# Optimization experiments

Hardware: AMD Instinct MI355X
Metric: run time of the kernel (lower is better)

The kernel has to match this reference:

```python
import jax, jax.numpy as jnp
import numpy as np

NUM_HEADS = 16
HEAD_DIM = 64
MEMORY_SIZE = 65536
K_SIMILAR = 8
K_CONTIGUOUS = 2
SURPRISE_THRESHOLD = 0.5
EPS = 1e-8  # torch F.cosine_similarity eps


def setup_inputs() -> dict:
    key = jax.random.key(0)
    ks = jax.random.split(key, 6)
    B, H, S, HD = 4, NUM_HEADS, 8192, HEAD_DIM
    D = H * HD
    inputs = jax.random.normal(ks[0], (B, S, D), dtype=jnp.float32)
    q = jax.random.normal(ks[1], (B, H, S, HD), dtype=jnp.float32)
    k = jax.random.normal(ks[2], (B, H, S, HD), dtype=jnp.float32)
    v = jax.random.normal(ks[3], (B, H, S, HD), dtype=jnp.float32)
    attention_mask = jnp.ones((B, S), dtype=jnp.float32)
    events = jax.random.normal(ks[4], (MEMORY_SIZE, D), dtype=jnp.float32)
    return {"inputs": inputs, "q": q, "k": k, "v": v,
            "attention_mask": attention_mask, "events": events,
            "seq_len_q": 8192}


def _segment_mean(kf, seg, S):
    # kf: [S, D], seg: [S] int32 segment ids (exclusive cumsum of boundary mask)
    sums = jax.ops.segment_sum(kf, seg, num_segments=S)          # [S, D]
    cnts = jax.ops.segment_sum(jnp.ones_like(seg, jnp.float32), seg, num_segments=S)
    means = sums / jnp.maximum(cnts, 1.0)[:, None]
    return means, cnts


def reference(inputs, q, k, v, attention_mask, events, seq_len_q):
    B, H, S, HD = k.shape
    D = H * HD
    # flatten keys per token: [B, S, H*HD]
    kf = k.transpose(0, 2, 1, 3).reshape(B, S, D)

    # --- surprise scores: ||k_t - k_{t-1}|| padded with 0 at t=0 ---
    diffs = kf[:, 1:] - kf[:, :-1]
    norms = jnp.linalg.norm(diffs, axis=-1)                      # [B, S-1]
    surprise = jnp.pad(norms, ((0, 0), (1, 0)))                  # [B, S]

    # --- event segmentation (threshold = mean + c*std, unbiased std like torch) ---
    mean = jnp.mean(surprise, axis=1, keepdims=True)
    std = jnp.std(surprise, axis=1, ddof=1, keepdims=True)
    bmask = surprise > (mean + SURPRISE_THRESHOLD * std)
    bmask = bmask.at[:, -1].set(True)                            # last index is always a boundary
    bi = bmask.astype(jnp.int32)
    seg = jnp.cumsum(bi, axis=1) - bi                            # token t -> #boundaries before t

    # --- memory update: mean-pool keys within each event (scatter) ---
    new_events, event_lengths = jax.vmap(_segment_mean, in_axes=(0, 0, None))(kf, seg, S)
    # new_events: [B, S, D] (rows >= num_events are zero), event_lengths: [B, S]

    # --- retrieval: cosine sim of last-token key vs memory, top-k gather ---
    query = kf[:, -1]                                            # [B, D]
    qn = jnp.maximum(jnp.linalg.norm(query, axis=-1), EPS)       # [B]
    en = jnp.maximum(jnp.linalg.norm(events, axis=-1), EPS)      # [M]
    sims = (query @ events.T) / (qn[:, None] * en[None, :])      # [B, M]
    kt = min(K_SIMILAR + K_CONTIGUOUS, events.shape[0])
    _, idx = jax.lax.top_k(sims, kt)                             # [B, kt]

    ret = events[idx]                                            # [B, kt, D]
    ret = ret.reshape(B, kt, H, HD).transpose(0, 2, 1, 3)        # [B, H, kt, HD]
    ret_k, ret_v = ret, ret                                      # non-differential: v == k slice

    aug_k = jnp.concatenate([ret_k, k], axis=2)                  # [B, H, kt+S, HD]
    aug_v = jnp.concatenate([ret_v, v], axis=2)
    aug_mask = jnp.concatenate([jnp.ones((B, kt), attention_mask.dtype), attention_mask], axis=1)

    cp = seq_len_q - 1
    ret_pos = jnp.linspace(float(cp - kt), float(cp - 1), kt, dtype=jnp.float32)
    pos = jnp.arange(S, dtype=jnp.float32)
    aug_positions = jnp.broadcast_to(jnp.concatenate([ret_pos, pos]), (B, kt + S))

    return (inputs, q, aug_k, aug_v, aug_mask, aug_positions, new_events, event_lengths)
```

## Files before the change

### kernel.cpp

```cpp
#include <hip/hip_runtime.h>
#include <math.h>

#define BB 4
#define HH 16
#define SS 8192
#define HDD 64
#define DD 1024
#define MEM 65536
#define KT 10
#define AUGROWS (SS + KT)

static const long O0 = 0;
static const long O1 = 33554432;
static const long O2 = 67108864;
static const long O3 = 100704256;
static const long O4 = 134299648;
static const long O5 = 134332456;
static const long O6 = 134365264;
static const long O7 = 167919696;

#define WS_NEED_FUSED 5767168UL

#define N4REG 8388608L

typedef float __attribute__((ext_vector_type(4))) f4v;

static __device__ __forceinline__ void nt_store4(float4* p, float4 v) {
    f4v t; t.x = v.x; t.y = v.y; t.z = v.z; t.w = v.w;
    __builtin_nontemporal_store(t, (f4v*)p);
}
static __device__ __forceinline__ float4 nt_load4(const float4* p) {
    f4v t = __builtin_nontemporal_load((const f4v*)p);
    float4 v; v.x = t.x; v.y = t.y; v.z = t.z; v.w = t.w;
    return v;
}

#define COPY_BLOCKS 4096
#define SIMS_BLOCKS 4096
__global__ __launch_bounds__(256) void bigfused_kernel(
        const float4* __restrict__ in0, const float4* __restrict__ q,
        const float4* __restrict__ k4, const float4* __restrict__ v,
        const float4* __restrict__ events4, float4* __restrict__ out4,
        double* __restrict__ partial, float* __restrict__ sims, int do_part) {
    __shared__ float4 qls4[BB][256];
    int blk = blockIdx.x;
    int tid = threadIdx.x;
    if (blk < COPY_BLOCKS) {
        int band = blk >> 10;
        long i = ((long)(blk & 1023)) * 256 + tid;
        const long bstride = 1024L * 256;
        if (band == 0) {
            for (; i < N4REG; i += bstride)
                nt_store4(out4 + (O0 >> 2) + i, nt_load4(in0 + i));
        } else if (band == 1) {
            for (; i < N4REG; i += bstride)
                nt_store4(out4 + (O1 >> 2) + i, nt_load4(q + i));
        } else if (band == 3) {
            for (; i < N4REG; i += bstride) {
                long chunk = i >> 17;
                long r = i & 131071;
                nt_store4(out4 + (O3 >> 2) + chunk * 131232L + 160 + r,
                          nt_load4(v + i));
            }
        } else {
            for (; i < N4REG; i += bstride) {
                long chunk = i >> 17;
                long r = i & 131071;
                float4 cur = k4[i];
                out4[(O2 >> 2) + chunk * 131232L + 160 + r] = cur;
                if (do_part) {
                    int s = (int)(r >> 4);
                    if (s > 0) {
                        float4 pv = k4[i - 16];
                        double dx = (double)cur.x - (double)pv.x;
                        double dy = (double)cur.y - (double)pv.y;
                        double dz = (double)cur.z - (double)pv.z;
                        double dw = (double)cur.w - (double)pv.w;
                        double acc = dx * dx + dy * dy + dz * dz + dw * dw;
                        acc += __shfl_xor(acc, 1, 64);
                        acc += __shfl_xor(acc, 2, 64);
                        acc += __shfl_xor(acc, 4, 64);
                        acc += __shfl_xor(acc, 8, 64);
                        if ((tid & 15) == 0) {
                            int b = (int)(chunk >> 4);
                            int h = (int)(chunk & 15);
                            partial[((long)b * SS + s) * HH + h] = acc;
                        }
                    }
                }
            }
        }
    } else {
        for (int j = tid; j < BB * 256; j += 256) {
            int b = j >> 8;
            int f4i = j & 255;
            qls4[b][f4i] =
                k4[((long)(b * HH + (f4i >> 4)) * SS + (SS - 1)) * 16 + (f4i & 15)];
        }
        __syncthreads();
        int w = tid >> 6;
        int lane = tid & 63;
        long e0 = (long)(blk - COPY_BLOCKS) * 4 + w;
        for (int rr = 0; rr < 4; ++rr) {
            long e = e0 + (long)rr * (4 * SIMS_BLOCKS);
            const float4* er = events4 + e * 256;
            float en = 0.f, d0 = 0.f, d1 = 0.f, d2 = 0.f, d3 = 0.f;
#pragma unroll
            for (int it = 0; it < 4; ++it) {
                int j4 = lane + it * 64;
                float4 ev = nt_load4(er + j4);
                en += ev.x * ev.x + ev.y * ev.y + ev.z * ev.z + ev.w * ev.w;
                float4 q0 = qls4[0][j4];
                d0 += ev.x * q0.x + ev.y * q0.y + ev.z * q0.z + ev.w * q0.w;
                float4 q1 = qls4[1][j4];
                d1 += ev.x * q1.x + ev.y * q1.y + ev.z * q1.z + ev.w * q1.w;
                float4 q2 = qls4[2][j4];
                d2 += ev.x * q2.x + ev.y * q2.y + ev.z * q2.z + ev.w * q2.w;
                float4 q3 = qls4[3][j4];
                d3 += ev.x * q3.x + ev.y * q3.y + ev.z * q3.z + ev.w * q3.w;
            }
            for (int m = 32; m >= 1; m >>= 1) {
                en += __shfl_xor(en, m, 64);
                d0 += __shfl_xor(d0, m, 64);
                d1 += __shfl_xor(d1, m, 64);
                d2 += __shfl_xor(d2, m, 64);
                d3 += __shfl_xor(d3, m, 64);
            }
            if (lane == 0) {
                float enn = fmaxf(sqrtf(en), 1e-8f);
                sims[0 * (long)MEM + e] = d0 / enn;
                sims[1 * (long)MEM + e] = d1 / enn;
                sims[2 * (long)MEM + e] = d2 / enn;
                sims[3 * (long)MEM + e] = d3 / enn;
            }
        }
    }
}

__global__ __launch_bounds__(256) void surprise_fallback_kernel(
        const float* __restrict__ k, double* __restrict__ surprise) {
    int wid = (int)(((long)blockIdx.x * blockDim.x + threadIdx.x) >> 6);
    int lane = threadIdx.x & 63;
    if (wid >= BB * SS) return;
    int b = wid >> 13;
    int s = wid & (SS - 1);
    double acc = 0.0;
    if (s > 0) {
        const float* kb = k + (long)b * HH * SS * HDD;
        for (int h = 0; h < HH; ++h) {
            long off = ((long)h * SS + s) * HDD + lane;
            double d = (double)kb[off] - (double)kb[off - HDD];
            acc += d * d;
        }
        for (int m = 32; m >= 1; m >>= 1) acc += __shfl_xor(acc, m, 64);
    }
    if (lane == 0) surprise[wid] = (s == 0) ? 0.0 : sqrt(acc);
}

__global__ __launch_bounds__(1024) void postfused_kernel(
        const double* __restrict__ partial, double* __restrict__ surprise,
        int* __restrict__ bpos, int* __restrict__ nseg,
        const float* __restrict__ sims, float* __restrict__ cval,
        int* __restrict__ cidx, int* __restrict__ idxout,
        const float* __restrict__ amask, const void* __restrict__ seqp,
        float* __restrict__ out, int* __restrict__ counters, int fused) {
    __shared__ double sd[1024];
    __shared__ int si[1024];
    __shared__ float lv[256][KT];
    __shared__ int li[256][KT];
    int blk = blockIdx.x;
    int tid = threadIdx.x;

    if (blk < 32) {
        if (fused) {
            int t = blk * 1024 + tid;
            int s = t & (SS - 1);
            double acc = 0.0;
            if (s > 0) {
                const double* row = partial + (long)t * HH;
#pragma unroll
                for (int h = 0; h < HH; ++h) acc += row[h];
            }
            surprise[t] = (s == 0) ? 0.0 : sqrt(acc);
        }
        __threadfence();
        __syncthreads();
        if (tid == 0) atomicAdd(&counters[0], 1);
    } else if (blk < 36) {
        if (tid == 0) {
            while (atomicAdd(&counters[0], 0) < 32) __builtin_amdgcn_s_sleep(8);
        }
        __syncthreads();
        __threadfence();
        int b = blk - 32;
        const double* sp = surprise + (long)b * SS;
        double loc[8];
        double sum = 0.0;
        for (int j = 0; j < 8; ++j) { loc[j] = sp[tid * 8 + j]; sum += loc[j]; }
        sd[tid] = sum;
        __syncthreads();
        for (int off = 512; off >= 1; off >>= 1) {
            if (tid < off) sd[tid] += sd[tid + off];
            __syncthreads();
        }
        double mean = sd[0] / SS;
        __syncthreads();
        double vs = 0.0;
        for (int j = 0; j < 8; ++j) { double d = loc[j] - mean; vs += d * d; }
        sd[tid] = vs;
        __syncthreads();
        for (int off = 512; off >= 1; off >>= 1) {
            if (tid < off) sd[tid] += sd[tid + off];
            __syncthreads();
        }
        double thr = mean + 0.5 * sqrt(sd[0] / (SS - 1));
        __syncthreads();
        int bi[8];
        int cnt = 0;
        for (int j = 0; j < 8; ++j) {
            int s = tid * 8 + j;
            bi[j] = (s == SS - 1) || (loc[j] > thr);
            cnt += bi[j];
        }
        si[tid] = cnt;
        __syncthreads();
        for (int off = 1; off < 1024; off <<= 1) {
            int v = 0;
            if (tid >= off) v = si[tid - off];
            __syncthreads();
            si[tid] += v;
            __syncthreads();
        }
        int run = si[tid] - cnt;
        for (int j = 0; j < 8; ++j) {
            if (bi[j]) { bpos[(long)b * SS + run] = tid * 8 + j; ++run; }
        }
        if (tid == 1023) nseg[b] = si[1023];
    } else if (blk < 100) {
        int g = blk - 36;
        int b = g >> 4;
        int part = g & 15;
        if (tid < 256) {
            const float* sb = sims + (long)b * MEM + part * 4096;
            float val[KT];
            int idx[KT];
#pragma unroll
            for (int p = 0; p < KT; ++p) { val[p] = -INFINITY; idx[p] = 0x7fffffff; }
            for (int it = 0; it < 16; ++it) {
                int e = tid + it * 256;
                float v = sb[e];
                if (v > val[KT - 1]) {
#pragma unroll
                    for (int p = KT - 1; p >= 1; --p) {
                        if (v > val[p - 1]) {
                            val[p] = val[p - 1];
                            idx[p] = idx[p - 1];
                        } else {
                            val[p] = v;
                            idx[p] = e;
                            v = -INFINITY;
                        }
                    }
                    if (v != -INFINITY) { val[0] = v; idx[0] = e; }
                }
            }
#pragma unroll
            for (int p = 0; p < KT; ++p) { lv[tid][p] = val[p]; li[tid][p] = idx[p]; }
        }
        for (int off = 128; off >= 1; off >>= 1) {
            __syncthreads();
            if (tid < off) {
                float a_[KT], b_[KT], m_[KT];
                int ai_[KT], bi_[KT], mi_[KT];
#pragma unroll
                for (int p = 0; p < KT; ++p) {
                    a_[p] = lv[tid][p];
                    ai_[p] = li[tid][p];
                    b_[p] = lv[tid + off][p];
                    bi_[p] = li[tid + off][p];
                }
                int pa = 0, pb = 0;
#pragma unroll
                for (int p = 0; p < KT; ++p) {
                    bool ta = (a_[pa] > b_[pb]) ||
                              (a_[pa] == b_[pb] && ai_[pa] < bi_[pb]);
                    if (ta) { m_[p] = a_[pa]; mi_[p] = ai_[pa]; ++pa; }
                    else    { m_[p] = b_[pb]; mi_[p] = bi_[pb]; ++pb; }
                }
#pragma unroll
                for (int p = 0; p < KT; ++p) { lv[tid][p] = m_[p]; li[tid][p] = mi_[p]; }
            }
        }
        __syncthreads();
        if (tid == 0) {
#pragma unroll
            for (int p = 0; p < KT; ++p) {
                cval[g * KT + p] = lv[0][p];
                cidx[g * KT + p] = part * 4096 + li[0][p];
            }
        }
        __threadfence();
        __syncthreads();
        if (tid == 0) atomicAdd(&counters[1], 1);
    } else if (blk < 104) {
        if (tid == 0) {
            while (atomicAdd(&counters[1], 0) < 64) __builtin_amdgcn_s_sleep(8);
        }
        __syncthreads();
        __threadfence();
        int b = blk - 100;
        float mv = -INFINITY;
        int mi = 0x7fffffff;
        if (tid < 160) { mv = cval[b * 160 + tid]; mi = cidx[b * 160 + tid]; }
        if (tid < 256) { lv[tid][0] = mv; li[tid][0] = mi; }
        __syncthreads();
        if (tid == 0) {
            for (int p = 0; p < KT; ++p) {
                float best = -INFINITY;
                int bi = 0x7fffffff;
                int bslot = 0;
                for (int j = 0; j < 160; ++j) {
                    if (lv[j][0] > best || (lv[j][0] == best && li[j][0] < bi)) {
                        best = lv[j][0];
                        bi = li[j][0];
                        bslot = j;
                    }
                }
                idxout[b * KT + p] = bi;
                lv[bslot][0] = -INFINITY;
                li[bslot][0] = 0x7fffffff;
            }
        }
    } else {
        int iv = ((const int*)seqp)[0];
        int seqlen;
        if (iv > 0 && iv < (1 << 24)) seqlen = iv;
        else seqlen = (int)(((const float*)seqp)[0]);
        int cp = seqlen - 1;
        int n = BB * AUGROWS;
        int i = (blk - 104) * 1024 + tid;
        int stride = 16 * 1024;
        for (; i < n; i += stride) {
            int b = i / AUGROWS;
            int t = i - b * AUGROWS;
            out[O4 + i] = (t < KT) ? 1.0f : amask[(long)b * SS + t - KT];
            out[O5 + i] = (t < KT) ? (float)(cp - KT + t) : (float)(t - KT);
        }
    }
}

__global__ __launch_bounds__(256) void segtail_kernel(
        const float4* __restrict__ out4c, const int* __restrict__ bpos,
        const int* __restrict__ nseg, const float* __restrict__ events,
        const int* __restrict__ idxin, float* __restrict__ out) {
    int blk = blockIdx.x;
    int tid = threadIdx.x;
    float4* ne4 = (float4*)(out + O6);
    if (blk < BB * SS) {
        int b = blk >> 13;
        int j = blk & (SS - 1);
        int ns = nseg[b];
        float4* row = ne4 + ((long)b * SS + j) * 256;
        if (j >= ns) {
            nt_store4(row + tid, make_float4(0.f, 0.f, 0.f, 0.f));
            if (tid == 0) out[O7 + (long)b * SS + j] = 0.0f;
            return;
        }
        int start = (j == 0) ? 0 : bpos[(long)b * SS + j - 1] + 1;
        int end = bpos[(long)b * SS + j];
        const float4* kb = out4c + (O2 >> 2) +
                           ((long)(b * HH + (tid >> 4)) * AUGROWS + KT) * 16 +
                           (tid & 15);
        double a0 = 0.0, a1 = 0.0, a2 = 0.0, a3 = 0.0;
        for (int s = start; s <= end; ++s) {
            float4 x = kb[(long)s * 16];
            a0 += (double)x.x; a1 += (double)x.y; a2 += (double)x.z; a3 += (double)x.w;
        }
        double inv = 1.0 / (double)(end - start + 1);
        nt_store4(row + tid, make_float4((float)(a0 * inv), (float)(a1 * inv),
                                         (float)(a2 * inv), (float)(a3 * inv)));
        if (tid == 0) out[O7 + (long)b * SS + j] = (float)(end - start + 1);
    } else {
        int g = blk - BB * SS;
        int b = g / KT;
        int t = g % KT;
        int ev = idxin[b * KT + t];
        for (int c = 0; c < 4; ++c) {
            int j = tid + c * 256;
            float vv = events[(long)ev * DD + j];
            int h = j >> 6;
            int d = j & 63;
            long dst = (((long)b * HH + h) * AUGROWS + t) * HDD + d;
            out[O2 + dst] = vv;
            out[O3 + dst] = vv;
        }
    }
}

extern "C" void kernel_launch(void* const* d_in, const int* in_sizes, int n_in,
                              void* d_out, int out_size, void* d_ws, size_t ws_size,
                              hipStream_t stream) {
    const float* in_inputs = (const float*)d_in[0];
    const float* in_q = (const float*)d_in[1];
    const float* in_k = (const float*)d_in[2];
    const float* in_v = (const float*)d_in[3];
    const float* in_amask = (const float*)d_in[4];
    const float* in_events = (const float*)d_in[5];
    const void* in_seq = d_in[6];
    float* out = (float*)d_out;

    char* ws = (char*)d_ws;
    double* surprise = (double*)ws;
    float* sims = (float*)(ws + 262144);
    int* bpos = (int*)(ws + 1310720);
    int* nseg = (int*)(ws + 1441792);
    int* idxw = (int*)(ws + 1441824);
    float* cval = (float*)(ws + 1442304);
    int* cidx = (int*)(ws + 1444864);
    int* counters = (int*)(ws + 1447424);
    double* partial = (double*)(ws + 1572864);

    const int fused = (ws_size >= WS_NEED_FUSED) ? 1 : 0;

    hipMemsetAsync(counters, 0, 64, stream);
    bigfused_kernel<<<COPY_BLOCKS + SIMS_BLOCKS, 256, 0, stream>>>(
        (const float4*)in_inputs, (const float4*)in_q, (const float4*)in_k,
        (const float4*)in_v, (const float4*)in_events, (float4*)out, partial,
        sims, fused);
    if (!fused)
        surprise_fallback_kernel<<<8192, 256, 0, stream>>>(in_k, surprise);
    postfused_kernel<<<120, 1024, 0, stream>>>(
        partial, surprise, bpos, nseg, sims, cval, cidx, idxw, in_amask,
        in_seq, out, counters, fused);
    segtail_kernel<<<BB * SS + BB * KT, 256, 0, stream>>>(
        (const float4*)out, bpos, nseg, in_events, idxw, out);
}
```

Baseline: 431.1 us.

## Merge all stages into one persistent kernel with software grid barriers

Replaces the three launches (copy/sims, post-processing, segment tail) with a single persistent kernel of 768 blocks. The stages are separated by atomic-counter grid barriers, and fixed-size blocks walk each stage in grid-stride loops. It also transposes the partial-surprise layout so the reduction reads are coalesced, and it mean-pools straight from the input keys instead of re-reading the output copy. This removes launch gaps and the spin-waits between kernels. In exchange it relies on all blocks being co-resident and has fewer waves in flight during the bandwidth-bound copy and segment phases.

```diff
diff --git a/kernel.cpp b/kernel.cpp
--- a/kernel.cpp
+++ b/kernel.cpp
@@ -22,6 +22,9 @@
 #define WS_NEED_FUSED 5767168UL
 
 #define N4REG 8388608L
+#define NB 768
+#define NTH 256
+#define GSTRIDE ((long)NB * NTH)
 
 typedef float __attribute__((ext_vector_type(4))) f4v;
 
@@ -35,106 +38,19 @@
     return v;
 }
 
-#define COPY_BLOCKS 4096
-#define SIMS_BLOCKS 4096
-__global__ __launch_bounds__(256) void bigfused_kernel(
-        const float4* __restrict__ in0, const float4* __restrict__ q,
-        const float4* __restrict__ k4, const float4* __restrict__ v,
-        const float4* __restrict__ events4, float4* __restrict__ out4,
-        double* __restrict__ partial, float* __restrict__ sims, int do_part) {
-    __shared__ float4 qls4[BB][256];
-    int blk = blockIdx.x;
-    int tid = threadIdx.x;
-    if (blk < COPY_BLOCKS) {
-        int band = blk >> 10;
-        long i = ((long)(blk & 1023)) * 256 + tid;
-        const long bstride = 1024L * 256;
-        if (band == 0) {
-            for (; i < N4REG; i += bstride)
-                nt_store4(out4 + (O0 >> 2) + i, nt_load4(in0 + i));
-        } else if (band == 1) {
-            for (; i < N4REG; i += bstride)
-                nt_store4(out4 + (O1 >> 2) + i, nt_load4(q + i));
-        } else if (band == 3) {
-            for (; i < N4REG; i += bstride) {
-                long chunk = i >> 17;
-                long r = i & 131071;
-                nt_store4(out4 + (O3 >> 2) + chunk * 131232L + 160 + r,
-                          nt_load4(v + i));
-            }
+static __device__ __forceinline__ void gbar(int* cnt, int* gen) {
+    __syncthreads();
+    __threadfence();
+    if (threadIdx.x == 0) {
+        int g = atomicAdd(gen, 0);
+        if (atomicAdd(cnt, 1) == NB - 1) {
+            atomicAdd(gen, 1);
         } else {
-            for (; i < N4REG; i += bstride) {
-                long chunk = i >> 17;
-                long r = i & 131071;
-                float4 cur = k4[i];
-                out4[(O2 >> 2) + chunk * 131232L + 160 + r] = cur;
-                if (do_part) {
-                    int s = (int)(r >> 4);
-                    if (s > 0) {
-                        float4 pv = k4[i - 16];
-                        double dx = (double)cur.x - (double)pv.x;
-                        double dy = (double)cur.y - (double)pv.y;
-                        double dz = (double)cur.z - (double)pv.z;
-                        double dw = (double)cur.w - (double)pv.w;
-                        double acc = dx * dx + dy * dy + dz * dz + dw * dw;
-                        acc += __shfl_xor(acc, 1, 64);
-                        acc += __shfl_xor(acc, 2, 64);
-                        acc += __shfl_xor(acc, 4, 64);
-                        acc += __shfl_xor(acc, 8, 64);
-                        if ((tid & 15) == 0) {
-                            int b = (int)(chunk >> 4);
-                            int h = (int)(chunk & 15);
-                            partial[((long)b * SS + s) * HH + h] = acc;
-                        }
-                    }
-                }
-            }
-        }
-    } else {
-        for (int j = tid; j < BB * 256; j += 256) {
-            int b = j >> 8;
-            int f4i = j & 255;
-            qls4[b][f4i] =
-                k4[((long)(b * HH + (f4i >> 4)) * SS + (SS - 1)) * 16 + (f4i & 15)];
-        }
-        __syncthreads();
-        int w = tid >> 6;
-        int lane = tid & 63;
-        long e0 = (long)(blk - COPY_BLOCKS) * 4 + w;
-        for (int rr = 0; rr < 4; ++rr) {
-            long e = e0 + (long)rr * (4 * SIMS_BLOCKS);
-            const float4* er = events4 + e * 256;
-            float en = 0.f, d0 = 0.f, d1 = 0.f, d2 = 0.f, d3 = 0.f;
-#pragma unroll
-            for (int it = 0; it < 4; ++it) {
-                int j4 = lane + it * 64;
-                float4 ev = nt_load4(er + j4);
-                en += ev.x * ev.x + ev.y * ev.y + ev.z * ev.z + ev.w * ev.w;
-                float4 q0 = qls4[0][j4];
-                d0 += ev.x * q0.x + ev.y * q0.y + ev.z * q0.z + ev.w * q0.w;
-                float4 q1 = qls4[1][j4];
-                d1 += ev.x * q1.x + ev.y * q1.y + ev.z * q1.z + ev.w * q1.w;
-                float4 q2 = qls4[2][j4];
-                d2 += ev.x * q2.x + ev.y * q2.y + ev.z * q2.z + ev.w * q2.w;
-                float4 q3 = qls4[3][j4];
-                d3 += ev.x * q3.x + ev.y * q3.y + ev.z * q3.z + ev.w * q3.w;
-            }
-            for (int m = 32; m >= 1; m >>= 1) {
-                en += __shfl_xor(en, m, 64);
-                d0 += __shfl_xor(d0, m, 64);
-                d1 += __shfl_xor(d1, m, 64);
-                d2 += __shfl_xor(d2, m, 64);
-                d3 += __shfl_xor(d3, m, 64);
-            }
-            if (lane == 0) {
-                float enn = fmaxf(sqrtf(en), 1e-8f);
-                sims[0 * (long)MEM + e] = d0 / enn;
-                sims[1 * (long)MEM + e] = d1 / enn;
-                sims[2 * (long)MEM + e] = d2 / enn;
-                sims[3 * (long)MEM + e] = d3 / enn;
-            }
-        }
-    }
+            while (atomicAdd(gen, 0) == g) __builtin_amdgcn_s_sleep(8);
+        }
+    }
+    __syncthreads();
+    __threadfence();
 }
 
 __global__ __launch_bounds__(256) void surprise_fallback_kernel(
@@ -157,116 +73,161 @@
     if (lane == 0) surprise[wid] = (s == 0) ? 0.0 : sqrt(acc);
 }
 
-__global__ __launch_bounds__(1024) void postfused_kernel(
-        const double* __restrict__ partial, double* __restrict__ surprise,
-        int* __restrict__ bpos, int* __restrict__ nseg,
-        const float* __restrict__ sims, float* __restrict__ cval,
-        int* __restrict__ cidx, int* __restrict__ idxout,
-        const float* __restrict__ amask, const void* __restrict__ seqp,
-        float* __restrict__ out, int* __restrict__ counters, int fused) {
-    __shared__ double sd[1024];
-    __shared__ int si[1024];
-    __shared__ float lv[256][KT];
-    __shared__ int li[256][KT];
+__global__ __launch_bounds__(256, 4) void mega_kernel(
+        const float4* __restrict__ in0, const float4* __restrict__ q,
+        const float4* __restrict__ k4, const float4* __restrict__ v,
+        const float4* __restrict__ events4, const float* __restrict__ amask,
+        const void* __restrict__ seqp, float* __restrict__ out,
+        double* __restrict__ partial, double* __restrict__ surprise,
+        float* __restrict__ sims, int* __restrict__ bpos,
+        int* __restrict__ nseg, float* __restrict__ cval,
+        int* __restrict__ cidx, int* __restrict__ idxw,
+        int* __restrict__ counters, int fused) {
+    __shared__ __align__(16) char smem[20992];
     int blk = blockIdx.x;
     int tid = threadIdx.x;
-
-    if (blk < 32) {
-        if (fused) {
-            int t = blk * 1024 + tid;
+    int gtid = blk * NTH + tid;
+    float4* out4 = (float4*)out;
+    const float* eventsf = (const float*)events4;
+
+    for (long i = gtid; i < 4 * N4REG; i += GSTRIDE) {
+        int region = (int)(i >> 23);
+        long rel = i & (N4REG - 1);
+        if (region == 0) {
+            nt_store4(out4 + (O0 >> 2) + rel, nt_load4(in0 + rel));
+        } else if (region == 1) {
+            nt_store4(out4 + (O1 >> 2) + rel, nt_load4(q + rel));
+        } else if (region == 3) {
+            long chunk = rel >> 17;
+            long r = rel & 131071;
+            nt_store4(out4 + (O3 >> 2) + chunk * 131232L + 160 + r,
+                      nt_load4(v + rel));
+        } else {
+            long chunk = rel >> 17;
+            long r = rel & 131071;
+            float4 cur = k4[rel];
+            out4[(O2 >> 2) + chunk * 131232L + 160 + r] = cur;
+            if (fused) {
+                int s = (int)(r >> 4);
+                if (s > 0) {
+                    float4 pv = k4[rel - 16];
+                    double dx = (double)cur.x - (double)pv.x;
+                    double dy = (double)cur.y - (double)pv.y;
+                    double dz = (double)cur.z - (double)pv.z;
+                    double dw = (double)cur.w - (double)pv.w;
+                    double acc = dx * dx + dy * dy + dz * dz + dw * dw;
+                    acc += __shfl_xor(acc, 1, 64);
+                    acc += __shfl_xor(acc, 2, 64);
+                    acc += __shfl_xor(acc, 4, 64);
+                    acc += __shfl_xor(acc, 8, 64);
+                    if ((tid & 15) == 0)
+                        partial[chunk * SS + s] = acc;
+                }
+            }
+        }
+    }
+    {
+        float4(*qls4)[256] = (float4(*)[256])smem;
+        for (int j = tid; j < BB * 256; j += 256) {
+            int b = j >> 8;
+            int f4i = j & 255;
+            qls4[b][f4i] =
+                k4[((long)(b * HH + (f4i >> 4)) * SS + (SS - 1)) * 16 + (f4i & 15)];
+        }
+        __syncthreads();
+        int w = tid >> 6;
+        int lane = tid & 63;
+        for (long e = blk * 4 + w; e < MEM; e += NB * 4) {
+            const float4* er = events4 + e * 256;
+            float en = 0.f, d0 = 0.f, d1 = 0.f, d2 = 0.f, d3 = 0.f;
+#pragma unroll
+            for (int it = 0; it < 4; ++it) {
+                int j4 = lane + it * 64;
+                float4 ev = nt_load4(er + j4);
+                en += ev.x * ev.x + ev.y * ev.y + ev.z * ev.z + ev.w * ev.w;
+                float4 q0 = qls4[0][j4];
+                d0 += ev.x * q0.x + ev.y * q0.y + ev.z * q0.z + ev.w * q0.w;
+                float4 q1 = qls4[1][j4];
+                d1 += ev.x * q1.x + ev.y * q1.y + ev.z * q1.z + ev.w * q1.w;
+                float4 q2 = qls4[2][j4];
+                d2 += ev.x * q2.x + ev.y * q2.y + ev.z * q2.z + ev.w * q2.w;
+                float4 q3 = qls4[3][j4];
+                d3 += ev.x * q3.x + ev.y * q3.y + ev.z * q3.z + ev.w * q3.w;
+            }
+            for (int m = 32; m >= 1; m >>= 1) {
+                en += __shfl_xor(en, m, 64);
+                d0 += __shfl_xor(d0, m, 64);
+                d1 += __shfl_xor(d1, m, 64);
+                d2 += __shfl_xor(d2, m, 64);
+                d3 += __shfl_xor(d3, m, 64);
+            }
+            if (lane == 0) {
+                float enn = fmaxf(sqrtf(en), 1e-8f);
+                sims[0 * (long)MEM + e] = d0 / enn;
+                sims[1 * (long)MEM + e] = d1 / enn;
+                sims[2 * (long)MEM + e] = d2 / enn;
+                sims[3 * (long)MEM + e] = d3 / enn;
+            }
+        }
+    }
+    {
+        int iv = ((const int*)seqp)[0];
+        int seqlen = (iv > 0 && iv < (1 << 24)) ? iv
+                                                : (int)(((const float*)seqp)[0]);
+        int cp = seqlen - 1;
+        for (int i = gtid; i < BB * AUGROWS; i += (int)GSTRIDE) {
+            int b = i / AUGROWS;
+            int t = i - b * AUGROWS;
+            out[O4 + i] = (t < KT) ? 1.0f : amask[(long)b * SS + t - KT];
+            out[O5 + i] = (t < KT) ? (float)(cp - KT + t) : (float)(t - KT);
+        }
+    }
+    gbar(&counters[0], &counters[1]);
+
+    if (fused) {
+        for (int t = gtid; t < BB * SS; t += (int)GSTRIDE) {
             int s = t & (SS - 1);
+            int b = t >> 13;
             double acc = 0.0;
             if (s > 0) {
-                const double* row = partial + (long)t * HH;
-#pragma unroll
-                for (int h = 0; h < HH; ++h) acc += row[h];
+#pragma unroll
+                for (int h = 0; h < HH; ++h)
+                    acc += partial[(((long)(b * HH + h)) << 13) + s];
             }
             surprise[t] = (s == 0) ? 0.0 : sqrt(acc);
         }
-        __threadfence();
-        __syncthreads();
-        if (tid == 0) atomicAdd(&counters[0], 1);
-    } else if (blk < 36) {
-        if (tid == 0) {
-            while (atomicAdd(&counters[0], 0) < 32) __builtin_amdgcn_s_sleep(8);
-        }
-        __syncthreads();
-        __threadfence();
-        int b = blk - 32;
-        const double* sp = surprise + (long)b * SS;
-        double loc[8];
-        double sum = 0.0;
-        for (int j = 0; j < 8; ++j) { loc[j] = sp[tid * 8 + j]; sum += loc[j]; }
-        sd[tid] = sum;
-        __syncthreads();
-        for (int off = 512; off >= 1; off >>= 1) {
-            if (tid < off) sd[tid] += sd[tid + off];
-            __syncthreads();
-        }
-        double mean = sd[0] / SS;
-        __syncthreads();
-        double vs = 0.0;
-        for (int j = 0; j < 8; ++j) { double d = loc[j] - mean; vs += d * d; }
-        sd[tid] = vs;
-        __syncthreads();
-        for (int off = 512; off >= 1; off >>= 1) {
-            if (tid < off) sd[tid] += sd[tid + off];
-            __syncthreads();
-        }
-        double thr = mean + 0.5 * sqrt(sd[0] / (SS - 1));
-        __syncthreads();
-        int bi[8];
-        int cnt = 0;
-        for (int j = 0; j < 8; ++j) {
-            int s = tid * 8 + j;
-            bi[j] = (s == SS - 1) || (loc[j] > thr);
-            cnt += bi[j];
-        }
-        si[tid] = cnt;
-        __syncthreads();
-        for (int off = 1; off < 1024; off <<= 1) {
-            int v = 0;
-            if (tid >= off) v = si[tid - off];
-            __syncthreads();
-            si[tid] += v;
-            __syncthreads();
-        }
-        int run = si[tid] - cnt;
-        for (int j = 0; j < 8; ++j) {
-            if (bi[j]) { bpos[(long)b * SS + run] = tid * 8 + j; ++run; }
-        }
-        if (tid == 1023) nseg[b] = si[1023];
-    } else if (blk < 100) {
-        int g = blk - 36;
+    }
+    if (blk >= 128 && blk < 192) {
+        int g = blk - 128;
         int b = g >> 4;
         int part = g & 15;
-        if (tid < 256) {
-            const float* sb = sims + (long)b * MEM + part * 4096;
-            float val[KT];
-            int idx[KT];
-#pragma unroll
-            for (int p = 0; p < KT; ++p) { val[p] = -INFINITY; idx[p] = 0x7fffffff; }
-            for (int it = 0; it < 16; ++it) {
-                int e = tid + it * 256;
-                float v = sb[e];
-                if (v > val[KT - 1]) {
-#pragma unroll
-                    for (int p = KT - 1; p >= 1; --p) {
-                        if (v > val[p - 1]) {
-                            val[p] = val[p - 1];
-                            idx[p] = idx[p - 1];
-                        } else {
-                            val[p] = v;
-                            idx[p] = e;
-                            v = -INFINITY;
-                        }
+        const float* sb = sims + (long)b * MEM + part * 4096;
+        float(*lv)[KT] = (float(*)[KT])smem;
+        int(*li)[KT] = (int(*)[KT])(smem + 10240);
+        float val[KT];
+        int idx[KT];
+#pragma unroll
+        for (int p = 0; p < KT; ++p) { val[p] = -INFINITY; idx[p] = 0x7fffffff; }
+        for (int it = 0; it < 16; ++it) {
+            int e = tid + it * 256;
+            float vv = sb[e];
+            if (vv > val[KT - 1]) {
+#pragma unroll
+                for (int p = KT - 1; p >= 1; --p) {
+                    if (vv > val[p - 1]) {
+                        val[p] = val[p - 1];
+                        idx[p] = idx[p - 1];
+                    } else {
+                        val[p] = vv;
+                        idx[p] = e;
+                        vv = -INFINITY;
                     }
-                    if (v != -INFINITY) { val[0] = v; idx[0] = e; }
-                }
-            }
-#pragma unroll
-            for (int p = 0; p < KT; ++p) { lv[tid][p] = val[p]; li[tid][p] = idx[p]; }
-        }
+                }
+                if (vv != -INFINITY) { val[0] = vv; idx[0] = e; }
+            }
+        }
+#pragma unroll
+        for (int p = 0; p < KT; ++p) { lv[tid][p] = val[p]; li[tid][p] = idx[p]; }
         for (int off = 128; off >= 1; off >>= 1) {
             __syncthreads();
             if (tid < off) {
@@ -299,20 +260,81 @@
                 cidx[g * KT + p] = part * 4096 + li[0][p];
             }
         }
-        __threadfence();
-        __syncthreads();
-        if (tid == 0) atomicAdd(&counters[1], 1);
-    } else if (blk < 104) {
-        if (tid == 0) {
-            while (atomicAdd(&counters[1], 0) < 64) __builtin_amdgcn_s_sleep(8);
-        }
-        __syncthreads();
-        __threadfence();
-        int b = blk - 100;
-        float mv = -INFINITY;
-        int mi = 0x7fffffff;
-        if (tid < 160) { mv = cval[b * 160 + tid]; mi = cidx[b * 160 + tid]; }
-        if (tid < 256) { lv[tid][0] = mv; li[tid][0] = mi; }
+    }
+    gbar(&counters[2], &counters[3]);
+
+    if (blk < 4) {
+        int b = blk;
+        const double* sp = surprise + (long)b * SS;
+        double* sd = (double*)smem;
+        int* si = (int*)(smem + 8192);
+        for (int p = 0; p < 4; ++p) {
+            int vt = tid + 256 * p;
+            double sum = 0.0;
+            for (int j = 0; j < 8; ++j) sum += sp[vt * 8 + j];
+            sd[vt] = sum;
+        }
+        __syncthreads();
+        for (int off = 512; off >= 1; off >>= 1) {
+            for (int p = 0; p < 4; ++p) {
+                int vt = tid + 256 * p;
+                if (vt < off) sd[vt] += sd[vt + off];
+            }
+            __syncthreads();
+        }
+        double mean = sd[0] / SS;
+        __syncthreads();
+        for (int p = 0; p < 4; ++p) {
+            int vt = tid + 256 * p;
+            double vs = 0.0;
+            for (int j = 0; j < 8; ++j) {
+                double d = sp[vt * 8 + j] - mean;
+                vs += d * d;
+            }
+            sd[vt] = vs;
+        }
+        __syncthreads();
+        for (int off = 512; off >= 1; off >>= 1) {
+            for (int p = 0; p < 4; ++p) {
+                int vt = tid + 256 * p;
+                if (vt < off) sd[vt] += sd[vt + off];
+            }
+            __syncthreads();
+        }
+        double thr = mean + 0.5 * sqrt(sd[0] / (SS - 1));
+        __syncthreads();
+        int s0 = tid * 32;
+        int cnt = 0;
+        for (int j = 0; j < 32; ++j) {
+            int s = s0 + j;
+            cnt += (s == SS - 1) || (sp[s] > thr);
+        }
+        si[tid] = cnt;
+        __syncthreads();
+        for (int off = 1; off < 256; off <<= 1) {
+            int vv = 0;
+            if (tid >= off) vv = si[tid - off];
+            __syncthreads();
+            si[tid] += vv;
+            __syncthreads();
+        }
+        int run = si[tid] - cnt;
+        for (int j = 0; j < 32; ++j) {
+            int s = s0 + j;
+            if ((s == SS - 1) || (sp[s] > thr)) {
+                bpos[(long)b * SS + run] = s;
+                ++run;
+            }
+        }
+        if (tid == 255) nseg[b] = si[255];
+    } else if (blk < 8) {
+        int b = blk - 4;
+        float* mv = (float*)smem;
+        int* mi = (int*)(smem + 1024);
+        if (tid < 160) {
+            mv[tid] = cval[b * 160 + tid];
+            mi[tid] = cidx[b * 160 + tid];
+        }
         __syncthreads();
         if (tid == 0) {
             for (int p = 0; p < KT; ++p) {
@@ -320,79 +342,65 @@
                 int bi = 0x7fffffff;
                 int bslot = 0;
                 for (int j = 0; j < 160; ++j) {
-                    if (lv[j][0] > best || (lv[j][0] == best && li[j][0] < bi)) {
-                        best = lv[j][0];
-                        bi = li[j][0];
+                    if (mv[j] > best || (mv[j] == best && mi[j] < bi)) {
+                        best = mv[j];
+                        bi = mi[j];
                         bslot = j;
                     }
                 }
-                idxout[b * KT + p] = bi;
-                lv[bslot][0] = -INFINITY;
-                li[bslot][0] = 0x7fffffff;
-            }
-        }
-    } else {
-        int iv = ((const int*)seqp)[0];
-        int seqlen;
-        if (iv > 0 && iv < (1 << 24)) seqlen = iv;
-        else seqlen = (int)(((const float*)seqp)[0]);
-        int cp = seqlen - 1;
-        int n = BB * AUGROWS;
-        int i = (blk - 104) * 1024 + tid;
-        int stride = 16 * 1024;
-        for (; i < n; i += stride) {
-            int b = i / AUGROWS;
-            int t = i - b * AUGROWS;
-            out[O4 + i] = (t < KT) ? 1.0f : amask[(long)b * SS + t - KT];
-            out[O5 + i] = (t < KT) ? (float)(cp - KT + t) : (float)(t - KT);
-        }
-    }
-}
-
-__global__ __launch_bounds__(256) void segtail_kernel(
-        const float4* __restrict__ out4c, const int* __restrict__ bpos,
-        const int* __restrict__ nseg, const float* __restrict__ events,
-        const int* __restrict__ idxin, float* __restrict__ out) {
-    int blk = blockIdx.x;
-    int tid = threadIdx.x;
-    float4* ne4 = (float4*)(out + O6);
-    if (blk < BB * SS) {
-        int b = blk >> 13;
-        int j = blk & (SS - 1);
-        int ns = nseg[b];
-        float4* row = ne4 + ((long)b * SS + j) * 256;
-        if (j >= ns) {
-            nt_store4(row + tid, make_float4(0.f, 0.f, 0.f, 0.f));
-            if (tid == 0) out[O7 + (long)b * SS + j] = 0.0f;
-            return;
-        }
-        int start = (j == 0) ? 0 : bpos[(long)b * SS + j - 1] + 1;
-        int end = bpos[(long)b * SS + j];
-        const float4* kb = out4c + (O2 >> 2) +
-                           ((long)(b * HH + (tid >> 4)) * AUGROWS + KT) * 16 +
-                           (tid & 15);
-        double a0 = 0.0, a1 = 0.0, a2 = 0.0, a3 = 0.0;
-        for (int s = start; s <= end; ++s) {
-            float4 x = kb[(long)s * 16];
-            a0 += (double)x.x; a1 += (double)x.y; a2 += (double)x.z; a3 += (double)x.w;
-        }
-        double inv = 1.0 / (double)(end - start + 1);
-        nt_store4(row + tid, make_float4((float)(a0 * inv), (float)(a1 * inv),
-                                         (float)(a2 * inv), (float)(a3 * inv)));
-        if (tid == 0) out[O7 + (long)b * SS + j] = (float)(end - start + 1);
-    } else {
-        int g = blk - BB * SS;
-        int b = g / KT;
-        int t = g % KT;
-        int ev = idxin[b * KT + t];
-        for (int c = 0; c < 4; ++c) {
-            int j = tid + c * 256;
-            float vv = events[(long)ev * DD + j];
-            int h = j >> 6;
-            int d = j & 63;
-            long dst = (((long)b * HH + h) * AUGROWS + t) * HDD + d;
-            out[O2 + dst] = vv;
-            out[O3 + dst] = vv;
+                idxw[b * KT + p] = bi;
+                mv[bslot] = -INFINITY;
+                mi[bslot] = 0x7fffffff;
+            }
+        }
+    }
+    gbar(&counters[4], &counters[5]);
+
+    const float4 z4 = make_float4(0.f, 0.f, 0.f, 0.f);
+    for (int slot = blk; slot < BB * SS + BB * KT; slot += NB) {
+        if (slot < BB * SS) {
+            int b = slot >> 13;
+            int j = slot & (SS - 1);
+            int ns = nseg[b];
+            float4* row = (float4*)(out + O6) + ((long)b * SS + j) * 256;
+            if (j >= ns) {
+                nt_store4(row + tid, z4);
+                if (tid == 0) out[O7 + (long)b * SS + j] = 0.0f;
+            } else {
+                int start = (j == 0) ? 0 : bpos[(long)b * SS + j - 1] + 1;
+                int end = bpos[(long)b * SS + j];
+                const float4* kb =
+                    k4 + ((long)(b * HH + (tid >> 4)) * SS) * 16 + (tid & 15);
+                double a0 = 0.0, a1 = 0.0, a2 = 0.0, a3 = 0.0;
+                for (int s = start; s <= end; ++s) {
+                    float4 x = kb[(long)s * 16];
+                    a0 += (double)x.x;
+                    a1 += (double)x.y;
+                    a2 += (double)x.z;
+                    a3 += (double)x.w;
+                }
+                double inv = 1.0 / (double)(end - start + 1);
+                nt_store4(row + tid,
+                          make_float4((float)(a0 * inv), (float)(a1 * inv),
+                                      (float)(a2 * inv), (float)(a3 * inv)));
+                if (tid == 0)
+                    out[O7 + (long)b * SS + j] = (float)(end - start + 1);
+            }
+        } else {
+            int g = slot - BB * SS;
+            int b = g / KT;
+            int t = g % KT;
+            int ev = idxw[b * KT + t];
+#pragma unroll
+            for (int c = 0; c < 4; ++c) {
+                int j = tid + c * 256;
+                float vv = eventsf[(long)ev * DD + j];
+                int h = j >> 6;
+                int d = j & 63;
+                long dst = (((long)b * HH + h) * AUGROWS + t) * HDD + d;
+                out[O2 + dst] = vv;
+                out[O3 + dst] = vv;
+            }
         }
     }
 }
@@ -423,15 +431,10 @@
     const int fused = (ws_size >= WS_NEED_FUSED) ? 1 : 0;
 
     hipMemsetAsync(counters, 0, 64, stream);
-    bigfused_kernel<<<COPY_BLOCKS + SIMS_BLOCKS, 256, 0, stream>>>(
-        (const float4*)in_inputs, (const float4*)in_q, (const float4*)in_k,
-        (const float4*)in_v, (const float4*)in_events, (float4*)out, partial,
-        sims, fused);
     if (!fused)
         surprise_fallback_kernel<<<8192, 256, 0, stream>>>(in_k, surprise);
-    postfused_kernel<<<120, 1024, 0, stream>>>(
-        partial, surprise, bpos, nseg, sims, cval, cidx, idxw, in_amask,
-        in_seq, out, counters, fused);
-    segtail_kernel<<<BB * SS + BB * KT, 256, 0, stream>>>(
-        (const float4*)out, bpos, nseg, in_events, idxw, out);
-}
+    mega_kernel<<<NB, NTH, 0, stream>>>(
+        (const float4*)in_inputs, (const float4*)in_q, (const float4*)in_k,
+        (const float4*)in_v, (const float4*)in_events, in_amask, in_seq, out,
+        partial, surprise, sims, bpos, nseg, cval, cidx, idxw, counters, fused);
+}
```

Measured after the change: 845.5 us. 1.96x slower.
